# Kernel tuning notes

Hardware: AMD Instinct MI355X
Metric: run time of the kernel (lower is better)

The kernel has to match this reference:

```python
import jax, jax.numpy as jnp
import numpy as np

DELTA_V = 0.5
DELTA_D = 3.0
PARAM_VAR = 1.0
PARAM_DIST = 1.0
PARAM_REG = 0.001
NUM_BIN_LABELS = 2   # binary labels in {0,1}
NUM_INST_LABELS = 6  # background + 5 lanes


def _disc_loss_single(pred, labels, num_labels, delta_v, delta_d):
    """pred: [D, N] float, labels: [N] int in [0, num_labels).
    Assumes all labels present (true w.h.p. for large N), so
    torch.unique(sorted=True) == arange(num_labels)."""
    D, N = pred.shape
    K = num_labels
    labels = labels.astype(jnp.int32)
    ones = jnp.ones((N,), dtype=pred.dtype)
    counts = jax.ops.segment_sum(ones, labels, num_segments=K)            # [K]
    sums = jax.ops.segment_sum(pred.T, labels, num_segments=K)            # [K, D]
    means = sums / counts[:, None]                                        # [K, D] segment means

    # variance (pull) term: distance of each pixel embedding to its segment mean
    mu_expand = means[labels]                                             # [N, D]
    dist = jnp.sqrt(jnp.sum((mu_expand - pred.T) ** 2, axis=1))           # [N]
    dist = jnp.maximum(dist - delta_v, 0.0) ** 2
    var_per_label = jax.ops.segment_sum(dist, labels, num_segments=K) / counts
    l_var = jnp.mean(var_per_label)

    # distance (push) term over all ordered pairs i != j of segment means
    diff = means[:, None, :] - means[None, :, :]                          # [K, K, D]
    sq = jnp.sum(diff ** 2, axis=-1)                                      # [K, K]
    offdiag = ~jnp.eye(K, dtype=bool)
    sq_safe = jnp.where(offdiag, sq, 1.0)  # avoid sqrt(0) grad NaN on diagonal
    dn = jnp.maximum(2.0 * delta_d - jnp.sqrt(sq_safe), 0.0) ** 2
    l_dist = jnp.sum(jnp.where(offdiag, dn, 0.0)) / (K * (K - 1))

    # regularizer: mean L2 norm of segment means (norm over feature dim)
    l_reg = jnp.mean(jnp.sqrt(jnp.sum(means ** 2, axis=1)))

    return PARAM_VAR * l_var + PARAM_DIST * l_dist + PARAM_REG * l_reg


def setup_inputs() -> dict:
    key = jax.random.key(0)
    k1, k2, k3, k4 = jax.random.split(key, 4)
    B, MN = 4, 512 * 1024
    return {
        "binary_logits": jax.random.normal(k1, (B, 2, MN), dtype=jnp.float32),
        "binary_labels": jax.random.randint(k2, (B, MN), 0, NUM_BIN_LABELS, dtype=jnp.int64),
        "instance_logits": jax.random.normal(k3, (B, 5, MN), dtype=jnp.float32),
        "instance_labels": jax.random.randint(k4, (B, MN), 0, NUM_INST_LABELS, dtype=jnp.int64),
    }


def reference(binary_logits, binary_labels, instance_logits, instance_labels):
    bin_loss_per = jax.vmap(
        lambda p, l: _disc_loss_single(p, l, NUM_BIN_LABELS, DELTA_V, DELTA_D)
    )(binary_logits, binary_labels)
    inst_loss_per = jax.vmap(
        lambda p, l: _disc_loss_single(p, l, NUM_INST_LABELS, DELTA_V, DELTA_D)
    )(instance_logits, instance_labels)
    return jnp.mean(bin_loss_per), jnp.mean(inst_loss_per)
```

## Files before the change

kernel.cpp:

```cpp
#include <hip/hip_runtime.h>
#include <math.h>

#define DELTA_V 0.5f
#define DELTA_D 3.0f
#define P_REG   0.001f
#define TPB     256
#define NVMAX   36

#define BPSB 128
#define BPSI 256
#define NBLK (4 * BPSB + 4 * BPSI)

#define P1_OFF    0
#define LBL_OFF   (P1_OFF + NVMAX * NBLK)
#define SCAL_OFF  (LBL_OFF + 2 * 524288)
#define P2_OFF    (SCAL_OFF + 64)

__device__ __forceinline__ int slice_base(int s) {
    return (s < 4) ? s * BPSB : 4 * BPSB + (s - 4) * BPSI;
}

template<int K, int D>
__device__ void pass1_body(const float* __restrict__ pred,
                           const int*  __restrict__ labels,
                           float* __restrict__ ws,
                           uchar4* __restrict__ lblPack,
                           int n4, int bx, int stride, int bid,
                           float (*lredW)[NVMAX]) {
    constexpr int NV = K * (D + 1);
    const float4* pred4 = (const float4*)pred;
    const int4*   lab4  = (const int4*)labels;

    float acc[K][D + 1];
    #pragma unroll
    for (int k = 0; k < K; ++k)
        #pragma unroll
        for (int j = 0; j <= D; ++j) acc[k][j] = 0.f;

    for (int i = bx * TPB + threadIdx.x; i < n4; i += stride) {
        int4 lv = lab4[i];
        int labs[4] = {lv.x, lv.y, lv.z, lv.w};
        lblPack[i] = make_uchar4((unsigned char)lv.x, (unsigned char)lv.y,
                                 (unsigned char)lv.z, (unsigned char)lv.w);
        float4 xv[D];
        #pragma unroll
        for (int d = 0; d < D; ++d) xv[d] = pred4[(size_t)d * n4 + i];
        const float* xs = (const float*)&xv[0];
        #pragma unroll
        for (int c = 0; c < 4; ++c) {
            const int lab = labs[c];
            #pragma unroll
            for (int k = 0; k < K; ++k) {
                const float ind = (lab == k) ? 1.f : 0.f;
                acc[k][D] += ind;
                #pragma unroll
                for (int d = 0; d < D; ++d)
                    acc[k][d] = fmaf(ind, xs[d * 4 + c], acc[k][d]);
            }
        }
    }

    const int wave = threadIdx.x >> 6, lane = threadIdx.x & 63;
    #pragma unroll
    for (int k = 0; k < K; ++k) {
        #pragma unroll
        for (int j = 0; j <= D; ++j) {
            float v = acc[k][j];
            for (int off = 32; off > 0; off >>= 1) v += __shfl_down(v, off);
            if (lane == 0) lredW[wave][k * (D + 1) + j] = v;
        }
    }
    __syncthreads();
    if (threadIdx.x < NV) {
        const int t = threadIdx.x;
        ws[P1_OFF + (size_t)t * NBLK + bid] =
            lredW[0][t] + lredW[1][t] + lredW[2][t] + lredW[3][t];
    }
}

__global__ __launch_bounds__(TPB)
void pass1_k(const float* __restrict__ bl, const int* __restrict__ bL,
             const float* __restrict__ il, const int* __restrict__ iL,
             float* __restrict__ ws, int MN) {
    __shared__ float lredW[4][NVMAX];
    const int bid = blockIdx.x, n4 = MN >> 2;
    uchar4* lblBase = (uchar4*)(ws + LBL_OFF);
    if (bid < 4 * BPSB) {
        const int s = bid / BPSB, bx = bid - s * BPSB;
        pass1_body<2, 2>(bl + (size_t)s * 2 * MN, bL + (size_t)s * MN,
                         ws, lblBase + (size_t)s * n4, n4, bx, BPSB * TPB, bid, lredW);
    } else {
        const int r = bid - 4 * BPSB;
        const int si = r / BPSI, bx = r - si * BPSI;
        pass1_body<6, 5>(il + (size_t)si * 5 * MN, iL + (size_t)si * MN,
                         ws, lblBase + (size_t)(4 + si) * n4, n4, bx, BPSI * TPB, bid, lredW);
    }
}

template<int K, int D, int NBP>
__device__ void pass2_slice(const float* __restrict__ pred,
                            const uchar4* __restrict__ lblPack,
                            float* __restrict__ ws,
                            const int s, const int bx, const int bid, const int n4) {
    constexpr int NV = K * (D + 1);
    __shared__ float tot[NVMAX];
    __shared__ float muS[30];
    __shared__ float cntS[6];
    __shared__ float lredW[4][6];
    const int t = threadIdx.x;
    const int sliceBase = bid - bx;

    if (t < NV) {
        const float* P = ws + P1_OFF + (size_t)t * NBLK + sliceBase;
        float v = 0.f;
        #pragma unroll 8
        for (int j = 0; j < NBP; ++j) v += P[j];
        tot[t] = v;
        const int k = t / (D + 1), jj = t - k * (D + 1);
        if (jj == D) cntS[k] = v;
    }
    __syncthreads();
    if (t < NV) {
        const int k = t / (D + 1), jj = t - k * (D + 1);
        if (jj < D) muS[k * D + jj] = tot[t] / cntS[k];
    }
    __syncthreads();

    if (bx == 0) {
        if (t < K) ws[SCAL_OFF + s * 8 + t] = cntS[t];
        if (t == 0) {
            float l_dist = 0.f, l_reg = 0.f;
            for (int i = 0; i < K; ++i) {
                float n2 = 0.f;
                for (int d = 0; d < D; ++d) n2 += muS[i * D + d] * muS[i * D + d];
                l_reg += sqrtf(n2);
                for (int j = 0; j < K; ++j) {
                    if (i == j) continue;
                    float sq = 0.f;
                    for (int d = 0; d < D; ++d) {
                        const float df = muS[i * D + d] - muS[j * D + d];
                        sq += df * df;
                    }
                    const float dn = fmaxf(2.f * DELTA_D - sqrtf(sq), 0.f);
                    l_dist += dn * dn;
                }
            }
            ws[SCAL_OFF + s * 8 + 6] =
                l_dist / (float)(K * (K - 1)) + P_REG * (l_reg / (float)K);
        }
    }

    const float4* pred4 = (const float4*)pred;

    float acc[K];
    #pragma unroll
    for (int k = 0; k < K; ++k) acc[k] = 0.f;

    const int stride = NBP * TPB;
    for (int i = bx * TPB + t; i < n4; i += stride) {
        const uchar4 lq = lblPack[i];
        int labs[4] = {lq.x, lq.y, lq.z, lq.w};
        float4 xv[D];
        #pragma unroll
        for (int d = 0; d < D; ++d) xv[d] = pred4[(size_t)d * n4 + i];
        const float* xs = (const float*)&xv[0];
        #pragma unroll
        for (int c = 0; c < 4; ++c) {
            const int lab = labs[c];
            float sq = 0.f;
            #pragma unroll
            for (int d = 0; d < D; ++d) {
                const float df = muS[lab * D + d] - xs[d * 4 + c];
                sq = fmaf(df, df, sq);
            }
            const float h = fmaxf(sqrtf(sq) - DELTA_V, 0.f);
            const float h2 = h * h;
            #pragma unroll
            for (int k = 0; k < K; ++k)
                acc[k] += (lab == k) ? h2 : 0.f;
        }
    }

    const int wave = t >> 6, lane = t & 63;
    #pragma unroll
    for (int k = 0; k < K; ++k) {
        float v = acc[k];
        for (int off = 32; off > 0; off >>= 1) v += __shfl_down(v, off);
        if (lane == 0) lredW[wave][k] = v;
    }
    __syncthreads();
    if (t < K)
        ws[P2_OFF + (size_t)t * NBLK + bid] =
            lredW[0][t] + lredW[1][t] + lredW[2][t] + lredW[3][t];
}

__global__ __launch_bounds__(TPB)
void pass2_k(const float* __restrict__ bl, const float* __restrict__ il,
             float* __restrict__ ws, int MN) {
    const int bid = blockIdx.x, n4 = MN >> 2;
    const uchar4* lblBase = (const uchar4*)(ws + LBL_OFF);
    if (bid < 4 * BPSB) {
        const int s = bid / BPSB, bx = bid - s * BPSB;
        pass2_slice<2, 2, BPSB>(bl + (size_t)s * 2 * MN, lblBase + (size_t)s * n4,
                                ws, s, bx, bid, n4);
    } else {
        const int r = bid - 4 * BPSB;
        const int si = r / BPSI, bx = r - si * BPSI;
        pass2_slice<6, 5, BPSI>(il + (size_t)si * 5 * MN, lblBase + (size_t)(4 + si) * n4,
                                ws, 4 + si, bx, bid, n4);
    }
}

__global__ void final_k(const float* __restrict__ ws, float* __restrict__ out) {
    __shared__ float contrib[48];
    const int t = threadIdx.x;
    if (t < 48) {
        const int s = t / 6, k = t - (t / 6) * 6;
        const int Ks = (s < 4) ? 2 : 6;
        const int NB = (s < 4) ? BPSB : BPSI;
        const int base = slice_base(s);
        float c = 0.f;
        if (k < Ks) {
            const float* P = ws + P2_OFF + (size_t)k * NBLK + base;
            float v = 0.f;
            #pragma unroll 8
            for (int j = 0; j < NB; ++j) v += P[j];
            c = v / ws[SCAL_OFF + s * 8 + k];
        }
        contrib[t] = c;
    }
    __syncthreads();
    if (t == 0) {
        float totB = 0.f, totI = 0.f;
        for (int s = 0; s < 8; ++s) {
            const int Ks = (s < 4) ? 2 : 6;
            float lv = 0.f;
            for (int k = 0; k < Ks; ++k) lv += contrib[s * 6 + k];
            lv /= (float)Ks;
            const float loss = lv + ws[SCAL_OFF + s * 8 + 6];
            if (s < 4) totB += loss; else totI += loss;
        }
        out[0] = totB * 0.25f;
        out[1] = totI * 0.25f;
    }
}

extern "C" void kernel_launch(void* const* d_in, const int* in_sizes, int n_in,
                              void* d_out, int out_size, void* d_ws, size_t ws_size,
                              hipStream_t stream) {
    const float* bl = (const float*)d_in[0];
    const int*   bL = (const int*)d_in[1];
    const float* il = (const float*)d_in[2];
    const int*   iL = (const int*)d_in[3];
    float* ws  = (float*)d_ws;
    float* out = (float*)d_out;

    const int B  = 4;
    const int MN = in_sizes[1] / B;

    pass1_k<<<dim3(NBLK), dim3(TPB), 0, stream>>>(bl, bL, il, iL, ws, MN);
    pass2_k<<<dim3(NBLK), dim3(TPB), 0, stream>>>(bl, il, ws, MN);
    final_k<<<dim3(1), dim3(64), 0, stream>>>(ws, out);
}
```

Measured before the change: 135.8 us.

## Fuse final reduction into pass2 via atomics and parallelize partial-sum reduction

Removes the final single-block kernel by having each pass2 block divide its per-label variance sums by the counts and atomically add its scaled contribution straight into the output. The output is zeroed in pass1. Pass2's prologue reduction of per-block pass1 partials is spread across thread groups with a shared-memory tree instead of a serial loop over up to 256 entries per thread. This saves a kernel launch and shortens the serial prologue, at the cost of float atomics that make the result order-dependent.

```diff
diff --git a/kernel.cpp b/kernel.cpp
--- a/kernel.cpp
+++ b/kernel.cpp
@@ -13,12 +13,6 @@
 
 #define P1_OFF    0
 #define LBL_OFF   (P1_OFF + NVMAX * NBLK)
-#define SCAL_OFF  (LBL_OFF + 2 * 524288)
-#define P2_OFF    (SCAL_OFF + 64)
-
-__device__ __forceinline__ int slice_base(int s) {
-    return (s < 4) ? s * BPSB : 4 * BPSB + (s - 4) * BPSI;
-}
 
 template<int K, int D>
 __device__ void pass1_body(const float* __restrict__ pred,
@@ -81,7 +75,9 @@
 __global__ __launch_bounds__(TPB)
 void pass1_k(const float* __restrict__ bl, const int* __restrict__ bL,
              const float* __restrict__ il, const int* __restrict__ iL,
-             float* __restrict__ ws, int MN) {
+             float* __restrict__ ws, float* __restrict__ out, int MN) {
+    if (blockIdx.x == 0 && threadIdx.x == 0) { out[0] = 0.f; out[1] = 0.f; }
+
     __shared__ float lredW[4][NVMAX];
     const int bid = blockIdx.x, n4 = MN >> 2;
     uchar4* lblBase = (uchar4*)(ws + LBL_OFF);
@@ -100,54 +96,59 @@
 template<int K, int D, int NBP>
 __device__ void pass2_slice(const float* __restrict__ pred,
                             const uchar4* __restrict__ lblPack,
-                            float* __restrict__ ws,
+                            const float* __restrict__ ws, float* __restrict__ out,
                             const int s, const int bx, const int bid, const int n4) {
     constexpr int NV = K * (D + 1);
-    __shared__ float tot[NVMAX];
+    constexpr int G  = TPB / NV;
+    __shared__ float red[G][NV];
     __shared__ float muS[30];
     __shared__ float cntS[6];
     __shared__ float lredW[4][6];
     const int t = threadIdx.x;
     const int sliceBase = bid - bx;
 
+    if (t < G * NV) {
+        const int g = t / NV, v = t - g * NV;
+        const float* P = ws + P1_OFF + (size_t)v * NBLK + sliceBase;
+        float sm = 0.f;
+        for (int j = g; j < NBP; j += G) sm += P[j];
+        red[g][v] = sm;
+    }
+    __syncthreads();
     if (t < NV) {
-        const float* P = ws + P1_OFF + (size_t)t * NBLK + sliceBase;
-        float v = 0.f;
-        #pragma unroll 8
-        for (int j = 0; j < NBP; ++j) v += P[j];
-        tot[t] = v;
+        float sm = 0.f;
+        #pragma unroll
+        for (int g = 0; g < G; ++g) sm += red[g][t];
         const int k = t / (D + 1), jj = t - k * (D + 1);
-        if (jj == D) cntS[k] = v;
+        if (jj == D) cntS[k] = sm;
+        else         red[0][t] = sm;
     }
     __syncthreads();
     if (t < NV) {
         const int k = t / (D + 1), jj = t - k * (D + 1);
-        if (jj < D) muS[k * D + jj] = tot[t] / cntS[k];
-    }
-    __syncthreads();
-
-    if (bx == 0) {
-        if (t < K) ws[SCAL_OFF + s * 8 + t] = cntS[t];
-        if (t == 0) {
-            float l_dist = 0.f, l_reg = 0.f;
-            for (int i = 0; i < K; ++i) {
-                float n2 = 0.f;
-                for (int d = 0; d < D; ++d) n2 += muS[i * D + d] * muS[i * D + d];
-                l_reg += sqrtf(n2);
-                for (int j = 0; j < K; ++j) {
-                    if (i == j) continue;
-                    float sq = 0.f;
-                    for (int d = 0; d < D; ++d) {
-                        const float df = muS[i * D + d] - muS[j * D + d];
-                        sq += df * df;
-                    }
-                    const float dn = fmaxf(2.f * DELTA_D - sqrtf(sq), 0.f);
-                    l_dist += dn * dn;
+        if (jj < D) muS[k * D + jj] = red[0][t] / cntS[k];
+    }
+    __syncthreads();
+
+    float ldr = 0.f;
+    if (bx == 0 && t == 0) {
+        float l_dist = 0.f, l_reg = 0.f;
+        for (int i = 0; i < K; ++i) {
+            float n2 = 0.f;
+            for (int d = 0; d < D; ++d) n2 += muS[i * D + d] * muS[i * D + d];
+            l_reg += sqrtf(n2);
+            for (int j = 0; j < K; ++j) {
+                if (i == j) continue;
+                float sq = 0.f;
+                for (int d = 0; d < D; ++d) {
+                    const float df = muS[i * D + d] - muS[j * D + d];
+                    sq += df * df;
                 }
+                const float dn = fmaxf(2.f * DELTA_D - sqrtf(sq), 0.f);
+                l_dist += dn * dn;
             }
-            ws[SCAL_OFF + s * 8 + 6] =
-                l_dist / (float)(K * (K - 1)) + P_REG * (l_reg / (float)K);
-        }
+        }
+        ldr = l_dist / (float)(K * (K - 1)) + P_REG * (l_reg / (float)K);
     }
 
     const float4* pred4 = (const float4*)pred;
@@ -189,59 +190,34 @@
         if (lane == 0) lredW[wave][k] = v;
     }
     __syncthreads();
-    if (t < K)
-        ws[P2_OFF + (size_t)t * NBLK + bid] =
-            lredW[0][t] + lredW[1][t] + lredW[2][t] + lredW[3][t];
+
+    if (t == 0) {
+        float contrib = 0.f;
+        #pragma unroll
+        for (int k = 0; k < K; ++k) {
+            const float sk = lredW[0][k] + lredW[1][k] + lredW[2][k] + lredW[3][k];
+            contrib += sk / cntS[k];
+        }
+        contrib *= 0.25f / (float)K;
+        contrib += 0.25f * ldr;
+        atomicAdd(out + ((s < 4) ? 0 : 1), contrib);
+    }
 }
 
 __global__ __launch_bounds__(TPB)
 void pass2_k(const float* __restrict__ bl, const float* __restrict__ il,
-             float* __restrict__ ws, int MN) {
+             const float* __restrict__ ws, float* __restrict__ out, int MN) {
     const int bid = blockIdx.x, n4 = MN >> 2;
     const uchar4* lblBase = (const uchar4*)(ws + LBL_OFF);
     if (bid < 4 * BPSB) {
         const int s = bid / BPSB, bx = bid - s * BPSB;
         pass2_slice<2, 2, BPSB>(bl + (size_t)s * 2 * MN, lblBase + (size_t)s * n4,
-                                ws, s, bx, bid, n4);
+                                ws, out, s, bx, bid, n4);
     } else {
         const int r = bid - 4 * BPSB;
         const int si = r / BPSI, bx = r - si * BPSI;
         pass2_slice<6, 5, BPSI>(il + (size_t)si * 5 * MN, lblBase + (size_t)(4 + si) * n4,
-                                ws, 4 + si, bx, bid, n4);
-    }
-}
-
-__global__ void final_k(const float* __restrict__ ws, float* __restrict__ out) {
-    __shared__ float contrib[48];
-    const int t = threadIdx.x;
-    if (t < 48) {
-        const int s = t / 6, k = t - (t / 6) * 6;
-        const int Ks = (s < 4) ? 2 : 6;
-        const int NB = (s < 4) ? BPSB : BPSI;
-        const int base = slice_base(s);
-        float c = 0.f;
-        if (k < Ks) {
-            const float* P = ws + P2_OFF + (size_t)k * NBLK + base;
-            float v = 0.f;
-            #pragma unroll 8
-            for (int j = 0; j < NB; ++j) v += P[j];
-            c = v / ws[SCAL_OFF + s * 8 + k];
-        }
-        contrib[t] = c;
-    }
-    __syncthreads();
-    if (t == 0) {
-        float totB = 0.f, totI = 0.f;
-        for (int s = 0; s < 8; ++s) {
-            const int Ks = (s < 4) ? 2 : 6;
-            float lv = 0.f;
-            for (int k = 0; k < Ks; ++k) lv += contrib[s * 6 + k];
-            lv /= (float)Ks;
-            const float loss = lv + ws[SCAL_OFF + s * 8 + 6];
-            if (s < 4) totB += loss; else totI += loss;
-        }
-        out[0] = totB * 0.25f;
-        out[1] = totI * 0.25f;
+                                ws, out, 4 + si, bx, bid, n4);
     }
 }
 
@@ -258,7 +234,6 @@
     const int B  = 4;
     const int MN = in_sizes[1] / B;
 
-    pass1_k<<<dim3(NBLK), dim3(TPB), 0, stream>>>(bl, bL, il, iL, ws, MN);
-    pass2_k<<<dim3(NBLK), dim3(TPB), 0, stream>>>(bl, il, ws, MN);
-    final_k<<<dim3(1), dim3(64), 0, stream>>>(ws, out);
-}
+    pass1_k<<<dim3(NBLK), dim3(TPB), 0, stream>>>(bl, bL, il, iL, ws, out, MN);
+    pass2_k<<<dim3(NBLK), dim3(TPB), 0, stream>>>(bl, il, ws, out, MN);
+}
```

Measured after the change: 148.8 us. 9.6% more time.
